# Kernel optimization log

Hardware: AMD Instinct MI355X
Metric: run time of the kernel (lower is better)

## Reference

```python
import jax, jax.numpy as jnp
import numpy as np

B, L, H, M, V = 8, 1024, 1024, 128, 32
LN_EPS = 1e-5


def setup_inputs() -> dict:
    key = jax.random.key(0)
    ks = jax.random.split(key, 6)
    x_enc = jax.random.normal(ks[0], (B, L, H), dtype=jnp.float32)
    ln_gamma = jnp.ones((H,), jnp.float32)
    ln_beta = jnp.zeros((H,), jnp.float32)
    Wq = jax.random.normal(ks[1], (H, H), jnp.float32) * 0.02
    Wk = jax.random.normal(ks[2], (H, H), jnp.float32) * 0.02
    W_embed = jax.random.normal(ks[3], (V * V, H), jnp.float32) * 0.02
    W_mlm = jax.random.normal(ks[4], (V, H), jnp.float32) * 0.02
    # masked positions per sequence: contiguous span [1, M] (token 0 at pos 0,
    # token 2 at pos M+1 in the original encoding); sorted, in-range, static M.
    mask_idx = jnp.tile(jnp.arange(1, M + 1, dtype=jnp.int32)[None, :], (B, 1))
    return {"x_enc": x_enc, "ln_gamma": ln_gamma, "ln_beta": ln_beta,
            "Wq": Wq, "Wk": Wk, "W_embed": W_embed, "W_mlm": W_mlm,
            "mask_idx": mask_idx}


def _layer_norm(x, gamma, beta):
    mu = jnp.mean(x, axis=-1, keepdims=True)
    var = jnp.mean(jnp.square(x - mu), axis=-1, keepdims=True)
    return (x - mu) * jax.lax.rsqrt(var + LN_EPS) * gamma + beta


def reference(x_enc, ln_gamma, ln_beta, Wq, Wk, W_embed, W_mlm, mask_idx):
    x = _layer_norm(x_enc, ln_gamma, ln_beta)            # [B,L,H]
    mlm_logits = jnp.einsum('blh,vh->blv', x, W_mlm)      # [B,L,V]

    # ragged masked-span gather (static M masked positions per sequence)
    masked_x = jnp.take_along_axis(x, mask_idx[:, :, None].astype(jnp.int32), axis=1)  # [B,M,H]
    q = jnp.einsum('bmh,oh->bmo', masked_x, Wq)           # fc_pmlm_q, no bias
    k = jnp.einsum('bmh,oh->bmo', masked_x, Wk)           # fc_pmlm_k, no bias
    pairs = jnp.einsum('bih,bjh->bijh', q, k)             # per-span outer product [B,M,M,H]
    pairs = pairs.reshape(B * M * M, H)
    logits = jnp.einsum('nh,vh->nv', pairs, W_embed)      # [B*M*M, V*V]

    diag_mask = jnp.tile(jnp.eye(M, dtype=bool).reshape(-1), B)  # [B*M*M]

    in_span = jnp.zeros((B, L), jnp.int8).at[jnp.arange(B)[:, None], mask_idx].set(1)
    mask_aa = in_span[:, :, None]                                      # [B,L,1]
    pair_mask_aa = (in_span[:, :, None] * in_span[:, None, :])[..., None]  # [B,L,L,1] int8

    return logits, mlm_logits, diag_mask, mask_aa, pair_mask_aa
```

## Files before the change

### kernel.cpp

```cpp
#include <hip/hip_runtime.h>


typedef float   f32x4 __attribute__((ext_vector_type(4)));
typedef _Float16 f16x8 __attribute__((ext_vector_type(8)));

__device__ __forceinline__ void gld16(const void* g, void* l) {
  __builtin_amdgcn_global_load_lds(
      (const __attribute__((address_space(1))) void*)g,
      (__attribute__((address_space(3))) void*)l, 16, 0, 0);
}

__global__ __launch_bounds__(256) void cvt_kernel(
    const float* __restrict__ wq, const float* __restrict__ wk,
    const float* __restrict__ we, const float* __restrict__ wm,
    _Float16* __restrict__ oq, _Float16* __restrict__ ok,
    _Float16* __restrict__ oe, _Float16* __restrict__ om) {
  int id = blockIdx.x * 256 + threadIdx.x;
  const float* src; _Float16* dst; int off;
  if (id < 262144)      { src = wq; dst = oq; off = id; }
  else if (id < 524288) { src = wk; dst = ok; off = id - 262144; }
  else if (id < 786432) { src = we; dst = oe; off = id - 524288; }
  else                  { src = wm; dst = om; off = id - 786432; }
  float4 v = ((const float4*)src)[off];
  union { _Float16 h[4]; uint2 u; } o;
  o.h[0] = (_Float16)v.x; o.h[1] = (_Float16)v.y;
  o.h[2] = (_Float16)v.z; o.h[3] = (_Float16)v.w;
  ((uint2*)dst)[off] = o.u;
}

__global__ __launch_bounds__(256) void ln_kernel(
    const float* __restrict__ x, const float* __restrict__ g,
    const float* __restrict__ be, _Float16* __restrict__ xo) {
  const int row = blockIdx.x, t = threadIdx.x;
  const float4 v = ((const float4*)(x + (size_t)row * 1024))[t];
  float s1 = v.x + v.y + v.z + v.w;
  float s2 = v.x * v.x + v.y * v.y + v.z * v.z + v.w * v.w;
  #pragma unroll
  for (int m = 1; m < 64; m <<= 1) {
    s1 += __shfl_xor(s1, m, 64);
    s2 += __shfl_xor(s2, m, 64);
  }
  __shared__ float red[8];
  const int w = t >> 6, lane = t & 63;
  if (lane == 0) { red[w * 2] = s1; red[w * 2 + 1] = s2; }
  __syncthreads();
  s1 = red[0] + red[2] + red[4] + red[6];
  s2 = red[1] + red[3] + red[5] + red[7];
  const float mu = s1 * (1.f / 1024.f);
  const float var = s2 * (1.f / 1024.f) - mu * mu;
  const float rs = rsqrtf(var + 1e-5f);
  const float4 gv = ((const float4*)g)[t];
  const float4 bv = ((const float4*)be)[t];
  union { _Float16 h[4]; uint2 u; } o;
  o.h[0] = (_Float16)((v.x - mu) * rs * gv.x + bv.x);
  o.h[1] = (_Float16)((v.y - mu) * rs * gv.y + bv.y);
  o.h[2] = (_Float16)((v.z - mu) * rs * gv.z + bv.z);
  o.h[3] = (_Float16)((v.w - mu) * rs * gv.w + bv.w);
  ((uint2*)(xo + (size_t)row * 1024))[t] = o.u;
}

__global__ __launch_bounds__(256, 4) void qk_gemm(
    const _Float16* __restrict__ xh, const _Float16* __restrict__ wq,
    const _Float16* __restrict__ wk, const int* __restrict__ midx,
    _Float16* __restrict__ qout, _Float16* __restrict__ kout) {
  __shared__ _Float16 at[64 * 32];
  __shared__ _Float16 bt[64 * 32];
  const int tid = threadIdx.x, w = tid >> 6, lane = tid & 63;
  const int l15 = lane & 15, quad = lane >> 4;
  const int ntile = blockIdx.x, rtile = blockIdx.y, mat = blockIdx.z;
  const _Float16* wmat = mat ? wk : wq;
  _Float16* outp = mat ? kout : qout;

  const int arow = tid >> 2;
  const int acol = (tid & 3) * 8;
  const int grow = rtile * 64 + arow;
  const int b = grow >> 7, m = grow & 127;
  const int src = midx[b * 128 + m];
  const _Float16* agp = xh + ((size_t)(b * 1024 + src)) * 1024 + acol;
  const _Float16* bgp = wmat + (size_t)(ntile * 64 + arow) * 1024 + acol;
  char* aldst = (char*)at + w * 1024;
  char* bldst = (char*)bt + w * 1024;

  f32x4 acc[4];
  const f32x4 zero = {0.f, 0.f, 0.f, 0.f};
  #pragma unroll
  for (int ns = 0; ns < 4; ++ns) acc[ns] = zero;

  for (int s = 0; s < 32; ++s) {
    const int kk = s * 32;
    gld16(agp + kk, aldst);
    gld16(bgp + kk, bldst);
    __syncthreads();
    const f16x8 af = *(const f16x8*)&at[(w * 16 + l15) * 32 + quad * 8];
    #pragma unroll
    for (int ns = 0; ns < 4; ++ns) {
      const f16x8 bf = *(const f16x8*)&bt[(ns * 16 + l15) * 32 + quad * 8];
      acc[ns] = __builtin_amdgcn_mfma_f32_16x16x32_f16(af, bf, acc[ns], 0, 0, 0);
    }
    __syncthreads();
  }
  #pragma unroll
  for (int ns = 0; ns < 4; ++ns) {
    const int col = ntile * 64 + ns * 16 + l15;
    #pragma unroll
    for (int r = 0; r < 4; ++r) {
      const int row = rtile * 64 + w * 16 + quad * 4 + r;
      outp[(size_t)row * 1024 + col] = (_Float16)acc[ns][r];
    }
  }
}

#define BG_BUF 49152
#define BG_WE  16384
#define BG_Q   147456
__global__ __launch_bounds__(512, 2) void big_gemm(
    const _Float16* __restrict__ qf, const _Float16* __restrict__ kf,
    const _Float16* __restrict__ wemb, float* __restrict__ out) {
  __shared__ __align__(16) char lds[151552];
  const int tid = threadIdx.x;
  const int w = tid >> 6, lane = tid & 63;
  const int l15 = lane & 15, quad = lane >> 4;
  const int wm = w >> 2, wn = w & 3;
  const int rtile = blockIdx.x;
  const int vtile = blockIdx.y;
  const int b = rtile >> 6;
  const int i0 = (rtile & 63) * 2;

  const int lrow = lane >> 3;
  const int cgsw = (lane & 7) ^ lrow;
  const char* kg = (const char*)(kf + (size_t)b * 128 * 1024);
  const char* wg = (const char*)(wemb + (size_t)vtile * 256 * 1024);
  const char* ks0 = kg + (size_t)(((w)      * 8 + lrow) * 2048 + cgsw * 16);
  const char* ks1 = kg + (size_t)(((w + 8)  * 8 + lrow) * 2048 + cgsw * 16);
  const char* ws0 = wg + (size_t)(((w)      * 8 + lrow) * 2048 + cgsw * 16);
  const char* ws1 = wg + (size_t)(((w + 8)  * 8 + lrow) * 2048 + cgsw * 16);
  const char* ws2 = wg + (size_t)(((w + 16) * 8 + lrow) * 2048 + cgsw * 16);
  const char* ws3 = wg + (size_t)(((w + 24) * 8 + lrow) * 2048 + cgsw * 16);
  const int kd0 = w * 1024,          kd1 = (w + 8) * 1024;
  const int wd0 = BG_WE + w * 1024,  wd1 = BG_WE + (w + 8) * 1024;
  const int wd2 = BG_WE + (w + 16) * 1024, wd3 = BG_WE + (w + 24) * 1024;

  const int swzb = (l15 & 7) << 4;
  const int col0 = (quad * 16) ^ swzb;
  const int col1 = (64 + quad * 16) ^ swzb;
  const int abase = l15 * 128;
  const int bbase = BG_WE + (wn * 64 + l15) * 128;
  const int qbase = BG_Q + wm * 2048 + quad * 16;

  if (w < 4) {
    const char* qsrc = (const char*)(qf + (size_t)(b * 128 + i0 + (w >> 1)) * 1024)
                       + (w & 1) * 1024 + lane * 16;
    gld16(qsrc, lds + BG_Q + w * 1024);
  }
  gld16(ks0, lds + kd0);              gld16(ks1, lds + kd1);
  gld16(ws0, lds + wd0);              gld16(ws1, lds + wd1);
  gld16(ws2, lds + wd2);              gld16(ws3, lds + wd3);
  gld16(ks0 + 128, lds + BG_BUF + kd0); gld16(ks1 + 128, lds + BG_BUF + kd1);
  gld16(ws0 + 128, lds + BG_BUF + wd0); gld16(ws1 + 128, lds + BG_BUF + wd1);
  gld16(ws2 + 128, lds + BG_BUF + wd2); gld16(ws3 + 128, lds + BG_BUF + wd3);

  f32x4 acc[8][4];
  #pragma unroll
  for (int a = 0; a < 8; ++a)
    #pragma unroll
    for (int c = 0; c < 4; ++c) acc[a][c] = (f32x4){0.f, 0.f, 0.f, 0.f};

  f16x8 af[4][2], bf0[2][2], bf1[2][2], qs0, qs1;

#define RD_A(mh)                                                               \
  _Pragma("unroll")                                                            \
  for (int ms = 0; ms < 4; ++ms) {                                             \
    af[ms][0] = *(const f16x8*)(lds + cb + abase + (mh) * 8192 + ms * 2048 + col0); \
    af[ms][1] = *(const f16x8*)(lds + cb + abase + (mh) * 8192 + ms * 2048 + col1); \
  }
#define RD_B(dst, nh)                                                          \
  _Pragma("unroll")                                                            \
  for (int ns = 0; ns < 2; ++ns) {                                             \
    dst[ns][0] = *(const f16x8*)(lds + cb + bbase + (nh) * 4096 + ns * 2048 + col0); \
    dst[ns][1] = *(const f16x8*)(lds + cb + bbase + (nh) * 4096 + ns * 2048 + col1); \
  }
#define MULT_A()                                                               \
  _Pragma("unroll")                                                            \
  for (int ms = 0; ms < 4; ++ms) { af[ms][0] *= qs0; af[ms][1] *= qs1; }
#define MFMA8(MH, NH, BFR)                                                     \
  __builtin_amdgcn_s_setprio(1);                                               \
  _Pragma("unroll")                                                            \
  for (int kh = 0; kh < 2; ++kh)                                               \
    _Pragma("unroll")                                                          \
    for (int ms = 0; ms < 4; ++ms)                                             \
      _Pragma("unroll")                                                        \
      for (int ns = 0; ns < 2; ++ns)                                           \
        acc[(MH) * 4 + ms][(NH) * 2 + ns] = __builtin_amdgcn_mfma_f32_16x16x32_f16( \
            af[ms][kh], BFR[ns][kh], acc[(MH) * 4 + ms][(NH) * 2 + ns], 0, 0, 0);   \
  __builtin_amdgcn_s_setprio(0);
#define BAR() __builtin_amdgcn_s_barrier()
#define LGKM0() asm volatile("s_waitcnt lgkmcnt(0)" ::: "memory")

  int cur = 0;
  #pragma unroll 1
  for (int t = 0; t < 16; ++t) {
    const int cb = cur * BG_BUF;
    int stg = cur + 2; if (stg >= 3) stg -= 3;
    const int sb = stg * BG_BUF;
    const int skb = (t + 2) * 128;
    const bool st = (t < 14);

    if (t < 15) asm volatile("s_waitcnt vmcnt(6)" ::: "memory");
    else        asm volatile("s_waitcnt vmcnt(0)" ::: "memory");
    BAR();

    qs0 = *(const f16x8*)(lds + qbase + t * 128);
    qs1 = *(const f16x8*)(lds + qbase + t * 128 + 64);
    RD_A(0)
    RD_B(bf0, 0)
    if (st) { gld16(ks0 + skb, lds + sb + kd0); gld16(ks1 + skb, lds + sb + kd1); }
    BAR(); LGKM0();
    MULT_A()
    MFMA8(0, 0, bf0)
    BAR();
    RD_B(bf1, 1)
    if (st) { gld16(ws0 + skb, lds + sb + wd0); gld16(ws1 + skb, lds + sb + wd1); }
    BAR(); LGKM0();
    MFMA8(0, 1, bf1)
    BAR();
    RD_A(1)
    if (st) { gld16(ws2 + skb, lds + sb + wd2); gld16(ws3 + skb, lds + sb + wd3); }
    BAR(); LGKM0();
    MULT_A()
    MFMA8(1, 1, bf1)
    BAR();
    BAR(); LGKM0();
    MFMA8(1, 0, bf0)
    BAR();

    cur = cur + 1; if (cur == 3) cur = 0;
  }

  const size_t nb = (size_t)((b * 128 + i0 + wm)) * 128;
  const int colb = vtile * 256 + wn * 64;
  #pragma unroll
  for (int ms = 0; ms < 8; ++ms) {
    #pragma unroll
    for (int ns = 0; ns < 4; ++ns) {
      #pragma unroll
      for (int r = 0; r < 4; ++r)
        out[(nb + ms * 16 + quad * 4 + r) * 1024 + colb + ns * 16 + l15] =
            acc[ms][ns][r];
    }
  }
#undef RD_A
#undef RD_B
#undef MULT_A
#undef MFMA8
#undef BAR
#undef LGKM0
}

__global__ __launch_bounds__(256) void mlm_kernel(
    const _Float16* __restrict__ xh, const _Float16* __restrict__ wm,
    float* __restrict__ out) {
  const int w = threadIdx.x >> 6, lane = threadIdx.x & 63;
  const int row = blockIdx.x * 4 + w;
  const int v = lane & 31, part = lane >> 5;
  const f16x8* xr = (const f16x8*)(xh + (size_t)row * 1024 + part * 512);
  const f16x8* wr = (const f16x8*)(wm + (size_t)v * 1024 + part * 512);
  float acc = 0.f;
  #pragma unroll 8
  for (int it = 0; it < 64; ++it) {
    const f16x8 p = xr[it] * wr[it];
    #pragma unroll
    for (int e = 0; e < 8; ++e) acc += (float)p[e];
  }
  acc += __shfl_xor(acc, 32, 64);
  if (part == 0) out[(size_t)row * 32 + v] = acc;
}

__global__ __launch_bounds__(256) void span_kernel(
    const int* __restrict__ midx, float* __restrict__ mask_aa,
    float* __restrict__ diag, float* __restrict__ span_ws) {
  __shared__ float flag[1024];
  const int b = blockIdx.x, t = threadIdx.x;
  for (int p = t; p < 1024; p += 256) flag[p] = 0.f;
  __syncthreads();
  if (t < 128) flag[midx[b * 128 + t]] = 1.f;
  __syncthreads();
  for (int p = t; p < 1024; p += 256) {
    const float f = flag[p];
    mask_aa[b * 1024 + p] = f;
    span_ws[b * 1024 + p] = f;
  }
  for (int p = t; p < 16384; p += 256)
    diag[b * 16384 + p] = ((p >> 7) == (p & 127)) ? 1.f : 0.f;
}

__global__ __launch_bounds__(256) void pairmask_kernel(
    const float* __restrict__ span_ws, float* __restrict__ out) {
  const int id = blockIdx.x * 256 + threadIdx.x;
  const int b = id >> 18;
  const int rem = id & 262143;
  const int i = rem >> 8;
  const int j4 = rem & 255;
  const float si = span_ws[b * 1024 + i];
  const float4 sj = ((const float4*)(span_ws + b * 1024))[j4];
  float4 o;
  o.x = si * sj.x; o.y = si * sj.y; o.z = si * sj.z; o.w = si * sj.w;
  ((float4*)out)[id] = o;
}

extern "C" void kernel_launch(void* const* d_in, const int* in_sizes, int n_in,
                              void* d_out, int out_size, void* d_ws, size_t ws_size,
                              hipStream_t stream) {
  const float* x_enc = (const float*)d_in[0];
  const float* gam   = (const float*)d_in[1];
  const float* bet   = (const float*)d_in[2];
  const float* Wq    = (const float*)d_in[3];
  const float* Wk    = (const float*)d_in[4];
  const float* We    = (const float*)d_in[5];
  const float* Wm    = (const float*)d_in[6];
  const int*   midx  = (const int*)d_in[7];
  float* out = (float*)d_out;

  char* ws = (char*)d_ws;
  _Float16* x_h  = (_Float16*)(ws);
  _Float16* q_h  = (_Float16*)(ws + ((size_t)16 << 20));
  _Float16* k_h  = (_Float16*)(ws + ((size_t)18 << 20));
  _Float16* wq_h = (_Float16*)(ws + ((size_t)20 << 20));
  _Float16* wk_h = (_Float16*)(ws + ((size_t)22 << 20));
  _Float16* we_h = (_Float16*)(ws + ((size_t)24 << 20));
  _Float16* wm_h = (_Float16*)(ws + ((size_t)26 << 20));
  float* span_ws = (float*)(ws + ((size_t)27 << 20));

  float* o_logits = out;
  float* o_mlm    = out + (size_t)134217728;
  float* o_diag   = o_mlm + 262144;
  float* o_maskaa = o_diag + 131072;
  float* o_pair   = o_maskaa + 8192;

  cvt_kernel<<<3104, 256, 0, stream>>>(Wq, Wk, We, Wm, wq_h, wk_h, we_h, wm_h);
  ln_kernel<<<8192, 256, 0, stream>>>(x_enc, gam, bet, x_h);
  qk_gemm<<<dim3(16, 16, 2), 256, 0, stream>>>(x_h, wq_h, wk_h, midx, q_h, k_h);
  big_gemm<<<dim3(512, 4), 512, 0, stream>>>(q_h, k_h, we_h, o_logits);
  mlm_kernel<<<2048, 256, 0, stream>>>(x_h, wm_h, o_mlm);
  span_kernel<<<8, 256, 0, stream>>>(midx, o_maskaa, o_diag, span_ws);
  pairmask_kernel<<<8192, 256, 0, stream>>>(span_ws, o_pair);
}
```

Baseline: 904.3 us.

## Make big_gemm persistent over 8 i-pairs per block with streamed q tiles

The big GEMM grid shrinks from 2048 blocks to 256. Each block now loops over 8 consecutive i-pairs (128 k-steps) for one vtile, writes results and clears the accumulators after each pair, and double-buffers the q rows in LDS, prefetching the next pair's q. The intent is to cut block launch and prologue/epilogue pipeline-fill costs and keep the 3-stage load pipeline running across tiles. It also merges the last two MFMA phases to drop a barrier pair and limits setprio to the MFMA sections. The cost is a single wave of 256 blocks, which may underfill the 256 CUs at 2 blocks/CU, plus stores serialized inside the loop.

```diff
diff --git a/kernel.cpp b/kernel.cpp
--- a/kernel.cpp
+++ b/kernel.cpp
@@ -111,20 +111,21 @@
 }
 
 #define BG_BUF 49152
+#define BG_Q   147456
 #define BG_WE  16384
-#define BG_Q   147456
 __global__ __launch_bounds__(512, 2) void big_gemm(
     const _Float16* __restrict__ qf, const _Float16* __restrict__ kf,
     const _Float16* __restrict__ wemb, float* __restrict__ out) {
-  __shared__ __align__(16) char lds[151552];
+  __shared__ __align__(16) char lds[155648];
   const int tid = threadIdx.x;
   const int w = tid >> 6, lane = tid & 63;
   const int l15 = lane & 15, quad = lane >> 4;
   const int wm = w >> 2, wn = w & 3;
-  const int rtile = blockIdx.x;
-  const int vtile = blockIdx.y;
-  const int b = rtile >> 6;
-  const int i0 = (rtile & 63) * 2;
+  const int bid = blockIdx.x;
+  const int vtile = bid & 3;
+  const int grp = bid >> 2;
+  const int b = grp >> 3;
+  const int i0base = (grp & 7) * 16;
 
   const int lrow = lane >> 3;
   const int cgsw = (lane & 7) ^ lrow;
@@ -140,18 +141,17 @@
   const int wd0 = BG_WE + w * 1024,  wd1 = BG_WE + (w + 8) * 1024;
   const int wd2 = BG_WE + (w + 16) * 1024, wd3 = BG_WE + (w + 24) * 1024;
 
+  const char* qsp = (const char*)(qf + (size_t)(b * 128 + i0base) * 1024)
+                    + (w >> 1) * 2048 + (w & 1) * 1024 + lane * 16;
+
   const int swzb = (l15 & 7) << 4;
   const int col0 = (quad * 16) ^ swzb;
   const int col1 = (64 + quad * 16) ^ swzb;
   const int abase = l15 * 128;
   const int bbase = BG_WE + (wn * 64 + l15) * 128;
-  const int qbase = BG_Q + wm * 2048 + quad * 16;
-
-  if (w < 4) {
-    const char* qsrc = (const char*)(qf + (size_t)(b * 128 + i0 + (w >> 1)) * 1024)
-                       + (w & 1) * 1024 + lane * 16;
-    gld16(qsrc, lds + BG_Q + w * 1024);
-  }
+  const int qrd = BG_Q + wm * 2048 + quad * 16;
+
+  if (w < 4) gld16(qsp, lds + BG_Q + w * 1024);
   gld16(ks0, lds + kd0);              gld16(ks1, lds + kd1);
   gld16(ws0, lds + wd0);              gld16(ws1, lds + wd1);
   gld16(ws2, lds + wd2);              gld16(ws3, lds + wd3);
@@ -183,7 +183,6 @@
   _Pragma("unroll")                                                            \
   for (int ms = 0; ms < 4; ++ms) { af[ms][0] *= qs0; af[ms][1] *= qs1; }
 #define MFMA8(MH, NH, BFR)                                                     \
-  __builtin_amdgcn_s_setprio(1);                                               \
   _Pragma("unroll")                                                            \
   for (int kh = 0; kh < 2; ++kh)                                               \
     _Pragma("unroll")                                                          \
@@ -191,61 +190,74 @@
       _Pragma("unroll")                                                        \
       for (int ns = 0; ns < 2; ++ns)                                           \
         acc[(MH) * 4 + ms][(NH) * 2 + ns] = __builtin_amdgcn_mfma_f32_16x16x32_f16( \
-            af[ms][kh], BFR[ns][kh], acc[(MH) * 4 + ms][(NH) * 2 + ns], 0, 0, 0);   \
-  __builtin_amdgcn_s_setprio(0);
+            af[ms][kh], BFR[ns][kh], acc[(MH) * 4 + ms][(NH) * 2 + ns], 0, 0, 0);
 #define BAR() __builtin_amdgcn_s_barrier()
 #define LGKM0() asm volatile("s_waitcnt lgkmcnt(0)" ::: "memory")
 
   int cur = 0;
   #pragma unroll 1
-  for (int t = 0; t < 16; ++t) {
+  for (int T = 0; T < 128; ++T) {
     const int cb = cur * BG_BUF;
     int stg = cur + 2; if (stg >= 3) stg -= 3;
     const int sb = stg * BG_BUF;
-    const int skb = (t + 2) * 128;
-    const bool st = (t < 14);
-
-    if (t < 15) asm volatile("s_waitcnt vmcnt(6)" ::: "memory");
-    else        asm volatile("s_waitcnt vmcnt(0)" ::: "memory");
+    const int j = T >> 4, tt = T & 15;
+    const int skb = ((T + 2) & 15) * 128;
+    const bool st = (T < 126);
+    const bool stq = (w < 4) && (((T + 2) & 15) == 0) && (T + 2 < 128);
+
+    if (T < 127) asm volatile("s_waitcnt vmcnt(6)" ::: "memory");
+    else         asm volatile("s_waitcnt vmcnt(0)" ::: "memory");
     BAR();
 
-    qs0 = *(const f16x8*)(lds + qbase + t * 128);
-    qs1 = *(const f16x8*)(lds + qbase + t * 128 + 64);
+    qs0 = *(const f16x8*)(lds + qrd + (j & 1) * 4096 + tt * 128);
+    qs1 = *(const f16x8*)(lds + qrd + (j & 1) * 4096 + tt * 128 + 64);
     RD_A(0)
     RD_B(bf0, 0)
+    if (stq) gld16(qsp + (T + 2) * 256,
+                   lds + BG_Q + ((((T + 2) >> 4) & 1) * 4096) + w * 1024);
     if (st) { gld16(ks0 + skb, lds + sb + kd0); gld16(ks1 + skb, lds + sb + kd1); }
     BAR(); LGKM0();
+    __builtin_amdgcn_s_setprio(1);
     MULT_A()
     MFMA8(0, 0, bf0)
+    __builtin_amdgcn_s_setprio(0);
     BAR();
     RD_B(bf1, 1)
     if (st) { gld16(ws0 + skb, lds + sb + wd0); gld16(ws1 + skb, lds + sb + wd1); }
     BAR(); LGKM0();
+    __builtin_amdgcn_s_setprio(1);
     MFMA8(0, 1, bf1)
+    __builtin_amdgcn_s_setprio(0);
     BAR();
     RD_A(1)
     if (st) { gld16(ws2 + skb, lds + sb + wd2); gld16(ws3 + skb, lds + sb + wd3); }
     BAR(); LGKM0();
+    __builtin_amdgcn_s_setprio(1);
     MULT_A()
     MFMA8(1, 1, bf1)
+    MFMA8(1, 0, bf0)
+    __builtin_amdgcn_s_setprio(0);
     BAR();
-    BAR(); LGKM0();
-    MFMA8(1, 0, bf0)
-    BAR();
 
     cur = cur + 1; if (cur == 3) cur = 0;
-  }
-
-  const size_t nb = (size_t)((b * 128 + i0 + wm)) * 128;
-  const int colb = vtile * 256 + wn * 64;
-  #pragma unroll
-  for (int ms = 0; ms < 8; ++ms) {
-    #pragma unroll
-    for (int ns = 0; ns < 4; ++ns) {
+
+    if (tt == 15) {
+      const size_t nb = (size_t)(b * 128 + i0base + 2 * j + wm) * 128;
+      const int colb = vtile * 256 + wn * 64;
       #pragma unroll
-      for (int r = 0; r < 4; ++r)
-        out[(nb + ms * 16 + quad * 4 + r) * 1024 + colb + ns * 16 + l15] =
-            acc[ms][ns][r];
+      for (int ms = 0; ms < 8; ++ms) {
+        #pragma unroll
+        for (int ns = 0; ns < 4; ++ns) {
+          #pragma unroll
+          for (int r = 0; r < 4; ++r)
+            out[(nb + ms * 16 + quad * 4 + r) * 1024 + colb + ns * 16 + l15] =
+                acc[ms][ns][r];
+        }
+      }
+      #pragma unroll
+      for (int a = 0; a < 8; ++a)
+        #pragma unroll
+        for (int c = 0; c < 4; ++c) acc[a][c] = (f32x4){0.f, 0.f, 0.f, 0.f};
     }
   }
 #undef RD_A
@@ -339,7 +351,7 @@
   cvt_kernel<<<3104, 256, 0, stream>>>(Wq, Wk, We, Wm, wq_h, wk_h, we_h, wm_h);
   ln_kernel<<<8192, 256, 0, stream>>>(x_enc, gam, bet, x_h);
   qk_gemm<<<dim3(16, 16, 2), 256, 0, stream>>>(x_h, wq_h, wk_h, midx, q_h, k_h);
-  big_gemm<<<dim3(512, 4), 512, 0, stream>>>(q_h, k_h, we_h, o_logits);
+  big_gemm<<<dim3(256), 512, 0, stream>>>(q_h, k_h, we_h, o_logits);
   mlm_kernel<<<2048, 256, 0, stream>>>(x_h, wm_h, o_mlm);
   span_kernel<<<8, 256, 0, stream>>>(midx, o_maskaa, o_diag, span_ws);
   pairmask_kernel<<<8192, 256, 0, stream>>>(span_ws, o_pair);
```

Measured after the change: 874.6 us. 1.03x faster.
